# Kernel tuning notes

Hardware: AMD Instinct MI355X
Metric: run time of the kernel (lower is better)

Reference implementation:

```python
import jax, jax.numpy as jnp
import numpy as np

# MMoE: E experts, each a 2-layer relu MLP (D->H0->H1); T softmax gates over experts.

def setup_inputs() -> dict:
    B, D, H0, H1, E, T = 16384, 1024, 1024, 512, 8, 2
    key = jax.random.key(0)
    ks = jax.random.split(key, 7)
    def glorot(k, shape, fan_in, fan_out):
        lim = jnp.sqrt(6.0 / (fan_in + fan_out)).astype(jnp.float32)
        return jax.random.uniform(k, shape, jnp.float32, -lim, lim)
    inputs = jax.random.normal(ks[0], (B, D), jnp.float32)
    W0 = glorot(ks[1], (E, D, H0), D, H0)      # expert layer 0 kernels
    b0 = jnp.zeros((E, H0), jnp.float32)
    W1 = glorot(ks[2], (E, H0, H1), H0, H1)    # expert layer 1 kernels
    b1 = jnp.zeros((E, H1), jnp.float32)
    Wg = glorot(ks[3], (T, D, E), D, E)        # gate kernels per task
    bg = jnp.zeros((T, E), jnp.float32)
    return {"inputs": inputs, "W0": W0, "b0": b0, "W1": W1, "b1": b1, "Wg": Wg, "bg": bg}


def reference(inputs, W0, b0, W1, b1, Wg, bg):
    # Experts: batched GEMMs over expert axis e.  h: [E, B, H]
    h = jax.nn.relu(jnp.einsum('bd,edh->ebh', inputs, W0) + b0[:, None, :])
    expert_out = jax.nn.relu(jnp.einsum('ebh,ehk->ebk', h, W1) + b1[:, None, :])  # [E, B, H1]
    # Gates: softmax over experts per task.  g: [T, B, E]
    gates = jax.nn.softmax(jnp.einsum('bd,tde->tbe', inputs, Wg) + bg[:, None, :], axis=-1)
    # Gate-weighted sum of expert outputs (einsum 'ai,ian->an' per task)
    outs = jnp.einsum('tbe,ebk->tbk', gates, expert_out)  # [T, B, H1]
    return tuple(outs[t] for t in range(outs.shape[0]))
```

## Files before the change

kernel.cpp:

```cpp
#include <hip/hip_runtime.h>

#define Bsz 16384
#define Dd  1024
#define H0d 1024
#define H1d 512
#define Ee  8
#define Tt  2

typedef short  s8_t  __attribute__((ext_vector_type(8)));
typedef float  fx4   __attribute__((ext_vector_type(4)));
typedef __bf16 bf8_t __attribute__((ext_vector_type(8)));

__device__ __forceinline__ ushort f2bf(float f) {
    uint u = __builtin_bit_cast(uint, f);
    uint r = u + 0x7fffu + ((u >> 16) & 1u);
    return (ushort)(r >> 16);
}
__device__ __forceinline__ float bf2f(ushort u) {
    uint x = ((uint)u) << 16;
    return __builtin_bit_cast(float, x);
}
__device__ __forceinline__ void gload16(const void* g, void* l) {
    __builtin_amdgcn_global_load_lds((const __attribute__((address_space(1))) uint*)g,
                                     (__attribute__((address_space(3))) uint*)l, 16, 0, 0);
}
__device__ __forceinline__ bf8_t ldbf8(const ushort* p) {
    s8_t v = *(const s8_t*)p;
    return __builtin_bit_cast(bf8_t, v);
}
__device__ __forceinline__ void barrier_mem() {
    asm volatile("" ::: "memory");
    __builtin_amdgcn_s_barrier();
    asm volatile("" ::: "memory");
}
#define VMCNT4() asm volatile("s_waitcnt vmcnt(4)" ::: "memory")
#define VMCNT2() asm volatile("s_waitcnt vmcnt(2)" ::: "memory")
#define VMCNT0() asm volatile("s_waitcnt vmcnt(0)" ::: "memory")

__global__ __launch_bounds__(256) void cvt_bf16_vec(const float* __restrict__ X,
                                                    ushort* __restrict__ Y, int n8) {
    int i = blockIdx.x * 256 + threadIdx.x;
    if (i >= n8) return;
    const float4* p = (const float4*)X + (size_t)i * 2;
    float4 a = p[0], b = p[1];
    s8_t o;
    o[0] = (short)f2bf(a.x); o[1] = (short)f2bf(a.y); o[2] = (short)f2bf(a.z); o[3] = (short)f2bf(a.w);
    o[4] = (short)f2bf(b.x); o[5] = (short)f2bf(b.y); o[6] = (short)f2bf(b.z); o[7] = (short)f2bf(b.w);
    ((s8_t*)Y)[i] = o;
}

__global__ __launch_bounds__(256) void transpose_cvt(const float* __restrict__ W,
                                                     ushort* __restrict__ WT, int R, int Cc) {
    __shared__ float tile[32][33];
    int e = blockIdx.z;
    int r0 = blockIdx.x * 32, c0 = blockIdx.y * 32;
    const float* Wp = W  + (size_t)e * R * Cc;
    ushort*      Tp = WT + (size_t)e * R * Cc;
    int tx = threadIdx.x, ty = threadIdx.y;
    #pragma unroll
    for (int i = 0; i < 32; i += 8)
        tile[ty + i][tx] = Wp[(size_t)(r0 + ty + i) * Cc + c0 + tx];
    __syncthreads();
    #pragma unroll
    for (int i = 0; i < 32; i += 8)
        Tp[(size_t)(c0 + ty + i) * R + r0 + tx] = f2bf(tile[tx][ty + i]);
}

__global__ __launch_bounds__(256) void transpose_wg(const float* __restrict__ Wg,
                                                    ushort* __restrict__ WgT) {
    int i = blockIdx.x * 256 + threadIdx.x;
    int d = i & 1023, r = i >> 10;
    int t = r >> 3, e = r & 7;
    WgT[i] = f2bf(Wg[((size_t)t * 1024 + d) * 8 + e]);
}

__global__ __launch_bounds__(256) void gates_mfma(const ushort* __restrict__ Xb,
                                                  const ushort* __restrict__ WgT,
                                                  const float* __restrict__ bg,
                                                  float* __restrict__ gts) {
    int wave = threadIdx.x >> 6, lane = threadIdx.x & 63;
    int base = blockIdx.x * 64 + wave * 16;
    int l15 = lane & 15, lhi = lane >> 4;
    fx4 acc0 = {}, acc1 = {};
    const ushort* xp = Xb  + (size_t)(base + l15) * Dd + lhi * 8;
    const ushort* wp = WgT + (size_t)l15 * Dd + lhi * 8;
    #pragma unroll
    for (int kt = 0; kt < 32; kt += 2) {
        bf8_t a0 = ldbf8(xp + kt * 32);
        bf8_t b0 = ldbf8(wp + kt * 32);
        bf8_t a1 = ldbf8(xp + kt * 32 + 32);
        bf8_t b1 = ldbf8(wp + kt * 32 + 32);
        acc0 = __builtin_amdgcn_mfma_f32_16x16x32_bf16(a0, b0, acc0, 0, 0, 0);
        acc1 = __builtin_amdgcn_mfma_f32_16x16x32_bf16(a1, b1, acc1, 0, 0, 0);
    }
    fx4 acc = acc0 + acc1;
    float bgv = bg[l15];
    int t = l15 >> 3, e = l15 & 7;
    #pragma unroll
    for (int r = 0; r < 4; ++r) {
        float v = acc[r] + bgv;
        float mx = v;
        mx = fmaxf(mx, __shfl_xor(mx, 1));
        mx = fmaxf(mx, __shfl_xor(mx, 2));
        mx = fmaxf(mx, __shfl_xor(mx, 4));
        float p = expf(v - mx);
        float s = p;
        s += __shfl_xor(s, 1); s += __shfl_xor(s, 2); s += __shfl_xor(s, 4);
        int row = base + lhi * 4 + r;
        gts[(size_t)t * Bsz * 8 + (size_t)row * 8 + e] = p / s;
    }
}

__global__ __launch_bounds__(512, 2) void gemm256(
    const ushort* __restrict__ A, const ushort* __restrict__ Bt,
    const float* __restrict__ bias, ushort* __restrict__ C,
    int N, int K, int nbn) {
    __shared__ ushort lds[65536];
    char* ldsc = (char*)lds;

    const int tid = threadIdx.x;
    const int wave = tid >> 6, lane = tid & 63;
    const int l15 = lane & 15, lhi = lane >> 4;
    const int wr = wave >> 2, wc = wave & 3;

    int nwg = gridDim.x, wg = blockIdx.x;
    int q = nwg >> 3;
    int swz = (wg & 7) * q + (wg >> 3);
    const int bm = (swz / nbn) * 256, bn = (swz % nbn) * 256;

    const int srcslot = (lane & 7) ^ (lane >> 3);
    const ushort* aSrc = A  + (size_t)(bm + (tid >> 3)) * K + srcslot * 8;
    const ushort* bSrc = Bt + (size_t)(bn + ((tid >> 8) << 6) + ((tid & 255) >> 3)) * K + srcslot * 8;
    const int sc0 = lhi ^ (l15 & 7);
    const int sc1 = (4 | lhi) ^ (l15 & 7);

    fx4 acc[8][4] = {};
    bf8_t aF[4][2], bF0[2][2], bF1[2][2];

    const int nK = K >> 6;
    int cur = 1;

#define STAGEA(U, KT)                                                                           \
    gload16(aSrc + (size_t)((U)*64) * K + (size_t)(KT)*64,                                      \
            ldsc + ((cur ^ 1) * 32768 + (U)*8192 + wave * 1024));                               \
    gload16(aSrc + (size_t)((U)*64 + 128) * K + (size_t)(KT)*64,                                \
            ldsc + ((cur ^ 1) * 32768 + (U)*8192 + 16384 + wave * 1024));
#define STAGEB(V, KT)                                                                           \
    gload16(bSrc + (size_t)((V)*32) * K + (size_t)(KT)*64,                                      \
            ldsc + (65536 + (cur ^ 1) * 32768 + (wave >> 2) * 8192 + (V)*4096 +                 \
                    (wave & 3) * 1024));                                                        \
    gload16(bSrc + (size_t)((V)*32 + 128) * K + (size_t)(KT)*64,                                \
            ldsc + (65536 + (cur ^ 1) * 32768 + (wave >> 2) * 8192 + (V)*4096 + 16384 +         \
                    (wave & 3) * 1024));

#define LDA(MH)                                                                                 \
    _Pragma("unroll") for (int m = 0; m < 4; ++m) {                                             \
        int Rb = cur * 32768 + (wr * 128 + (MH)*64 + m * 16 + l15) * 128;                       \
        aF[m][0] = ldbf8((const ushort*)(ldsc + Rb + sc0 * 16));                                \
        aF[m][1] = ldbf8((const ushort*)(ldsc + Rb + sc1 * 16));                                \
    }
#define LDB(NH, DST)                                                                            \
    _Pragma("unroll") for (int n = 0; n < 2; ++n) {                                             \
        int Rb = 65536 + cur * 32768 + (wc * 64 + (NH)*32 + n * 16 + l15) * 128;                \
        DST[n][0] = ldbf8((const ushort*)(ldsc + Rb + sc0 * 16));                               \
        DST[n][1] = ldbf8((const ushort*)(ldsc + Rb + sc1 * 16));                               \
    }
#define MM(MH, NH, BFR)                                                                         \
    __builtin_amdgcn_s_setprio(1);                                                              \
    _Pragma("unroll") for (int m = 0; m < 4; ++m)                                               \
    _Pragma("unroll") for (int n = 0; n < 2; ++n)                                               \
    _Pragma("unroll") for (int kk = 0; kk < 2; ++kk)                                            \
        acc[(MH)*4 + m][(NH)*2 + n] = __builtin_amdgcn_mfma_f32_16x16x32_bf16(                  \
            aF[m][kk], BFR[n][kk], acc[(MH)*4 + m][(NH)*2 + n], 0, 0, 0);                       \
    __builtin_amdgcn_s_setprio(0);

    STAGEA(0, 0); STAGEB(0, 0); STAGEB(1, 0); STAGEA(1, 0);

    for (int kt = 0; kt < nK - 1; ++kt) {
        cur = kt & 1;
        const int ks = kt + 1;
        VMCNT4(); barrier_mem();
        STAGEA(0, ks);
        LDA(0); LDB(0, bF0);
        MM(0, 0, bF0);
        VMCNT4(); barrier_mem();
        STAGEB(0, ks);
        LDB(1, bF1);
        MM(0, 1, bF1);
        VMCNT4(); barrier_mem();
        STAGEB(1, ks);
        LDA(1);
        MM(1, 1, bF1);
        barrier_mem();
        STAGEA(1, ks);
        MM(1, 0, bF0);
    }
    cur = (nK - 1) & 1;
    VMCNT4(); barrier_mem();
    LDA(0); LDB(0, bF0);
    MM(0, 0, bF0);
    VMCNT2(); barrier_mem();
    LDB(1, bF1);
    MM(0, 1, bF1);
    VMCNT0(); barrier_mem();
    LDA(1);
    MM(1, 1, bF1);
    MM(1, 0, bF0);

#undef STAGEA
#undef STAGEB
#undef LDA
#undef LDB
#undef MM

    float bv[4];
    #pragma unroll
    for (int ni = 0; ni < 4; ++ni) bv[ni] = bias[bn + wc * 64 + ni * 16 + l15];
    #pragma unroll
    for (int mi = 0; mi < 8; ++mi) {
        #pragma unroll
        for (int rr = 0; rr < 4; ++rr) {
            int row = bm + wr * 128 + mi * 16 + lhi * 4 + rr;
            ushort* cp = C + (size_t)row * N + bn + wc * 64 + l15;
            #pragma unroll
            for (int ni = 0; ni < 4; ++ni) {
                float v = acc[mi][ni][rr] + bv[ni];
                v = fmaxf(v, 0.f);
                cp[ni * 16] = f2bf(v);
            }
        }
    }
}

template <int MODE>
__global__ __launch_bounds__(256, 2) void gemm_bt(
    const ushort* __restrict__ A, const ushort* __restrict__ Bt,
    const float* __restrict__ bias, ushort* __restrict__ C,
    float* __restrict__ outAcc, const float* __restrict__ gts,
    int expert, int N, int K, int nbn) {
    __shared__ ushort Ash[128 * 64];
    __shared__ ushort Bsh[128 * 64];
    const int tid = threadIdx.x;
    const int wave = tid >> 6, lane = tid & 63;

    int nwg = gridDim.x, wg = blockIdx.x;
    int q = nwg >> 3;
    int swz = (wg & 7) * q + (wg >> 3);
    const int bm = (swz / nbn) * 128, bn = (swz % nbn) * 128;

    const int wm = (wave >> 1) * 64, wn = (wave & 1) * 64;
    const int l15 = lane & 15, lhi = lane >> 4;

    fx4 acc[4][4] = {};

    const int nK = K >> 6;
    for (int kt = 0; kt < nK; ++kt) {
        __syncthreads();
        #pragma unroll
        for (int i = 0; i < 4; ++i) {
            int c = (wave * 4 + i) * 64 + lane;
            int row = c >> 3, g = c & 7;
            const ushort* ga = A + (size_t)(bm + row) * K + kt * 64 + g * 8;
            gload16(ga, (char*)Ash + (wave * 4 + i) * 1024);
            const ushort* gb = Bt + (size_t)(bn + row) * K + kt * 64 + g * 8;
            gload16(gb, (char*)Bsh + (wave * 4 + i) * 1024);
        }
        __syncthreads();
        #pragma unroll
        for (int kk = 0; kk < 2; ++kk) {
            bf8_t af[4], bf_[4];
            #pragma unroll
            for (int m = 0; m < 4; ++m)
                af[m] = ldbf8((const ushort*)((const char*)Ash + (wm + m * 16 + l15) * 128 + kk * 64 + lhi * 16));
            #pragma unroll
            for (int n = 0; n < 4; ++n)
                bf_[n] = ldbf8((const ushort*)((const char*)Bsh + (wn + n * 16 + l15) * 128 + kk * 64 + lhi * 16));
            #pragma unroll
            for (int m = 0; m < 4; ++m)
                #pragma unroll
                for (int n = 0; n < 4; ++n)
                    acc[m][n] = __builtin_amdgcn_mfma_f32_16x16x32_bf16(af[m], bf_[n], acc[m][n], 0, 0, 0);
        }
    }

    #pragma unroll
    for (int m = 0; m < 4; ++m) {
        #pragma unroll
        for (int r = 0; r < 4; ++r) {
            int row = bm + wm + m * 16 + lhi * 4 + r;
            if (MODE == 0) {
                ushort* cp = C + (size_t)row * N + bn + wn + l15;
                #pragma unroll
                for (int n = 0; n < 4; ++n) {
                    float v = acc[m][n][r] + bias[bn + wn + n * 16 + l15];
                    v = fmaxf(v, 0.f);
                    cp[n * 16] = f2bf(v);
                }
            } else {
                float g0 = gts[(size_t)row * 8 + expert];
                float g1 = gts[(size_t)Bsz * 8 + (size_t)row * 8 + expert];
                #pragma unroll
                for (int n = 0; n < 4; ++n) {
                    int col = bn + wn + n * 16 + l15;
                    float v = acc[m][n][r] + bias[col];
                    v = fmaxf(v, 0.f);
                    float* o0 = outAcc + (size_t)row * N + col;
                    float* o1 = outAcc + (size_t)Bsz * N + (size_t)row * N + col;
                    *o0 += g0 * v;
                    *o1 += g1 * v;
                }
            }
        }
    }
}

__global__ __launch_bounds__(256) void combine_kernel(const ushort* __restrict__ eo,
                                                      const float* __restrict__ gts,
                                                      float* __restrict__ out) {
    int wave = threadIdx.x >> 6, lane = threadIdx.x & 63;
    int b = blockIdx.x * 4 + wave;
    float g0[8], g1[8];
    #pragma unroll
    for (int e = 0; e < 8; ++e) {
        g0[e] = gts[(size_t)b * 8 + e];
        g1[e] = gts[(size_t)Bsz * 8 + (size_t)b * 8 + e];
    }
    int k0 = lane * 8;
    float a0[8], a1[8];
    #pragma unroll
    for (int j = 0; j < 8; ++j) { a0[j] = 0.f; a1[j] = 0.f; }
    #pragma unroll
    for (int e = 0; e < 8; ++e) {
        s8_t v = *(const s8_t*)(eo + ((size_t)e * Bsz + b) * H1d + k0);
        #pragma unroll
        for (int j = 0; j < 8; ++j) {
            float f = bf2f((ushort)v[j]);
            a0[j] += g0[e] * f;
            a1[j] += g1[e] * f;
        }
    }
    float4* o0 = (float4*)(out + (size_t)b * H1d + k0);
    o0[0] = make_float4(a0[0], a0[1], a0[2], a0[3]);
    o0[1] = make_float4(a0[4], a0[5], a0[6], a0[7]);
    float4* o1 = (float4*)(out + (size_t)Bsz * H1d + (size_t)b * H1d + k0);
    o1[0] = make_float4(a1[0], a1[1], a1[2], a1[3]);
    o1[1] = make_float4(a1[4], a1[5], a1[6], a1[7]);
}

extern "C" void kernel_launch(void* const* d_in, const int* in_sizes, int n_in,
                              void* d_out, int out_size, void* d_ws, size_t ws_size,
                              hipStream_t stream) {
    const float* X  = (const float*)d_in[0];
    const float* W0 = (const float*)d_in[1];
    const float* b0 = (const float*)d_in[2];
    const float* W1 = (const float*)d_in[3];
    const float* b1 = (const float*)d_in[4];
    const float* Wg = (const float*)d_in[5];
    const float* bg = (const float*)d_in[6];
    float* out = (float*)d_out;

    size_t off = 0;
    auto alloc = [&](size_t bytes) {
        char* p = (char*)d_ws + off;
        off += (bytes + 255) & ~(size_t)255;
        return (void*)p;
    };
    ushort* Xb  = (ushort*)alloc((size_t)Bsz * Dd * 2);
    ushort* W0T = (ushort*)alloc((size_t)Ee * Dd * H0d * 2);
    ushort* W1T = (ushort*)alloc((size_t)Ee * H0d * H1d * 2);
    ushort* h   = (ushort*)alloc((size_t)Bsz * H0d * 2);
    float*  gts = (float*)alloc((size_t)Tt * Bsz * Ee * 4);
    ushort* WgT = (ushort*)alloc((size_t)Tt * Ee * Dd * 2);
    size_t eoBytes = (size_t)Ee * Bsz * H1d * 2;
    bool use_eo = (off + eoBytes) <= ws_size;
    ushort* eo = use_eo ? (ushort*)alloc(eoBytes) : nullptr;

    cvt_bf16_vec<<<(Bsz * Dd / 8 + 255) / 256, 256, 0, stream>>>(X, Xb, Bsz * Dd / 8);
    transpose_cvt<<<dim3(Dd / 32, H0d / 32, Ee), dim3(32, 8), 0, stream>>>(W0, W0T, Dd, H0d);
    transpose_cvt<<<dim3(H0d / 32, H1d / 32, Ee), dim3(32, 8), 0, stream>>>(W1, W1T, H0d, H1d);
    transpose_wg<<<(Tt * Ee * Dd) / 256, 256, 0, stream>>>(Wg, WgT);
    gates_mfma<<<Bsz / 64, 256, 0, stream>>>(Xb, WgT, bg, gts);
    if (!use_eo) hipMemsetAsync(d_out, 0, (size_t)out_size * sizeof(float), stream);

    for (int e = 0; e < Ee; ++e) {
        gemm256<<<dim3((Bsz / 256) * (H0d / 256)), 512, 0, stream>>>(
            Xb, W0T + (size_t)e * Dd * H0d, b0 + (size_t)e * H0d, h, H0d, Dd, H0d / 256);
        if (use_eo)
            gemm_bt<0><<<dim3((Bsz / 128) * (H1d / 128)), 256, 0, stream>>>(
                h, W1T + (size_t)e * H0d * H1d, b1 + (size_t)e * H1d,
                eo + (size_t)e * Bsz * H1d, nullptr, nullptr, e, H1d, H0d, H1d / 128);
        else
            gemm_bt<1><<<dim3((Bsz / 128) * (H1d / 128)), 256, 0, stream>>>(
                h, W1T + (size_t)e * H0d * H1d, b1 + (size_t)e * H1d,
                nullptr, out, gts, e, H1d, H0d, H1d / 128);
    }
    if (use_eo) combine_kernel<<<Bsz / 4, 256, 0, stream>>>(eo, gts, out);
}
```

Baseline: 575.3 us.

## Merge GEMM main loop into two phases and drop MFMA priority hints

Restructures the double-buffered GEMM K-loop from four staged sub-phases with barriers into two phases, issuing two global-to-LDS stages and three fragment loads before each pair of MFMA blocks. This cuts the barrier count per iteration and is meant to reduce synchronisation overhead. The s_setprio bracketing around MFMA blocks is also removed. The risks are less fine-grained overlap of loads with compute and the need for correct vmcnt accounting across the new stage grouping.

```diff
diff --git a/kernel.cpp b/kernel.cpp
--- a/kernel.cpp
+++ b/kernel.cpp
@@ -166,46 +166,33 @@
         DST[n][1] = ldbf8((const ushort*)(ldsc + Rb + sc1 * 16));                               \
     }
 #define MM(MH, NH, BFR)                                                                         \
-    __builtin_amdgcn_s_setprio(1);                                                              \
     _Pragma("unroll") for (int m = 0; m < 4; ++m)                                               \
     _Pragma("unroll") for (int n = 0; n < 2; ++n)                                               \
     _Pragma("unroll") for (int kk = 0; kk < 2; ++kk)                                            \
         acc[(MH)*4 + m][(NH)*2 + n] = __builtin_amdgcn_mfma_f32_16x16x32_bf16(                  \
-            aF[m][kk], BFR[n][kk], acc[(MH)*4 + m][(NH)*2 + n], 0, 0, 0);                       \
-    __builtin_amdgcn_s_setprio(0);
+            aF[m][kk], BFR[n][kk], acc[(MH)*4 + m][(NH)*2 + n], 0, 0, 0);
 
     STAGEA(0, 0); STAGEB(0, 0); STAGEB(1, 0); STAGEA(1, 0);
 
     for (int kt = 0; kt < nK - 1; ++kt) {
         cur = kt & 1;
         const int ks = kt + 1;
+        VMCNT2(); barrier_mem();
+        STAGEA(0, ks); STAGEB(0, ks);
+        LDA(0); LDB(0, bF0); LDB(1, bF1);
+        MM(0, 0, bF0); MM(0, 1, bF1);
         VMCNT4(); barrier_mem();
-        STAGEA(0, ks);
-        LDA(0); LDB(0, bF0);
-        MM(0, 0, bF0);
-        VMCNT4(); barrier_mem();
-        STAGEB(0, ks);
-        LDB(1, bF1);
-        MM(0, 1, bF1);
-        VMCNT4(); barrier_mem();
-        STAGEB(1, ks);
+        STAGEB(1, ks); STAGEA(1, ks);
         LDA(1);
-        MM(1, 1, bF1);
-        barrier_mem();
-        STAGEA(1, ks);
-        MM(1, 0, bF0);
+        MM(1, 1, bF1); MM(1, 0, bF0);
     }
     cur = (nK - 1) & 1;
-    VMCNT4(); barrier_mem();
-    LDA(0); LDB(0, bF0);
-    MM(0, 0, bF0);
     VMCNT2(); barrier_mem();
-    LDB(1, bF1);
-    MM(0, 1, bF1);
+    LDA(0); LDB(0, bF0); LDB(1, bF1);
+    MM(0, 0, bF0); MM(0, 1, bF1);
     VMCNT0(); barrier_mem();
     LDA(1);
-    MM(1, 1, bF1);
-    MM(1, 0, bF0);
+    MM(1, 1, bF1); MM(1, 0, bF0);
 
 #undef STAGEA
 #undef STAGEB
```

Measured after the change: 566.0 us. Within noise of the previous version (-1.6%).
